# Optimization experiments

Hardware: AMD Instinct MI355X
Metric: run time of the kernel (lower is better)

## Reference

```python
import jax, jax.numpy as jnp
import numpy as np

B, S, D_IN, D_OUT, H = 4, 2048, 1024, 1024, 16
HD = D_OUT // H


def setup_inputs() -> dict:
    key = jax.random.key(0)
    ks = jax.random.split(key, 6)
    sc_in = 1.0 / np.sqrt(D_IN)
    sc_out = 1.0 / np.sqrt(D_OUT)
    return {
        "x": jax.random.normal(ks[0], (B, S, D_IN), dtype=jnp.float32),
        "Wq": jax.random.normal(ks[1], (D_IN, D_OUT), dtype=jnp.float32) * sc_in,
        "Wk": jax.random.normal(ks[2], (D_IN, D_OUT), dtype=jnp.float32) * sc_in,
        "Wv": jax.random.normal(ks[3], (D_IN, D_OUT), dtype=jnp.float32) * sc_in,
        "Wo": jax.random.normal(ks[4], (D_OUT, D_OUT), dtype=jnp.float32) * sc_out,
        "bo": jax.random.normal(ks[5], (D_OUT,), dtype=jnp.float32) * 0.01,
    }


def reference(x, Wq, Wk, Wv, Wo, bo):
    b, s, _ = x.shape
    # projections -> [b, h, s, hd]
    def split_heads(t):
        return t.reshape(b, s, H, HD).transpose(0, 2, 1, 3)
    q = split_heads(x @ Wq)
    k = split_heads(x @ Wk)
    v = split_heads(x @ Wv)
    # full score matrix [b, h, s, s], causal mask, scaled softmax
    scores = jnp.einsum("bhqd,bhkd->bhqk", q, k)
    causal = jnp.tril(jnp.ones((s, s), dtype=bool))
    scores = jnp.where(causal, scores, -jnp.inf)
    attn = jax.nn.softmax(scores / np.sqrt(HD), axis=-1)
    # dropout p=0.0 -> identity
    ctx = jnp.einsum("bhqk,bhkd->bhqd", attn, v)
    ctx = ctx.transpose(0, 2, 1, 3).reshape(b, s, D_OUT)
    return ctx @ Wo + bo
```

## Files before the change

kernel.cpp:

```cpp
#include <hip/hip_runtime.h>


typedef float  f32x4  __attribute__((ext_vector_type(4)));
typedef __bf16 bf16x8 __attribute__((ext_vector_type(8)));
typedef __bf16 bf16x4 __attribute__((ext_vector_type(4)));

#define AS(n) __attribute__((address_space(n)))

__device__ __forceinline__ void gload16(const void* g, void* l) {
    __builtin_amdgcn_global_load_lds((const AS(1) void*)g, (AS(3) void*)l, 16, 0, 0);
}

__device__ __forceinline__ f32x4 mfma16(bf16x8 a, bf16x8 b, f32x4 c) {
    return __builtin_amdgcn_mfma_f32_16x16x32_bf16(a, b, c, 0, 0, 0);
}

__global__ void prep_kernel(const float4* __restrict__ x, __bf16* __restrict__ xb,
                            const float* __restrict__ Wq, const float* __restrict__ Wk,
                            const float* __restrict__ Wv, const float* __restrict__ Wo,
                            __bf16* __restrict__ wqkvt, __bf16* __restrict__ wot) {
    __shared__ float tile[32][33];
    int bid = blockIdx.x, tid = threadIdx.x;
    if (bid < 8192) {
        int t = bid * 256 + tid;
        float4 v = x[t];
        bf16x4 o = { (__bf16)v.x, (__bf16)v.y, (__bf16)v.z, (__bf16)v.w };
        ((bf16x4*)xb)[t] = o;
        return;
    }
    int idx = bid - 8192;
    int z = idx >> 10, rest = idx & 1023;
    int by = rest >> 5, bx = rest & 31;
    const float* src; __bf16* dst;
    if (z == 0)      { src = Wq; dst = wqkvt; }
    else if (z == 1) { src = Wk; dst = wqkvt + 1048576; }
    else if (z == 2) { src = Wv; dst = wqkvt + 2097152; }
    else             { src = Wo; dst = wot; }
    int tx = tid & 31, ty = tid >> 5;
    int xcol = bx * 32 + tx;
    int y0 = by * 32;
#pragma unroll
    for (int i = ty; i < 32; i += 8) tile[i][tx] = src[(size_t)(y0 + i) * 1024 + xcol];
    __syncthreads();
    int xo = by * 32 + tx;
    int yo0 = bx * 32;
#pragma unroll
    for (int i = ty; i < 32; i += 8) dst[(size_t)(yo0 + i) * 1024 + xo] = (__bf16)tile[tx][i];
}

__global__ __launch_bounds__(256, 2) void gemm_qkv_kernel(
        const __bf16* __restrict__ A, const __bf16* __restrict__ Bt,
        __bf16* __restrict__ Qp, __bf16* __restrict__ Kp, __bf16* __restrict__ Vt) {
    __shared__ __bf16 lA[128 * 32];
    __shared__ __bf16 lB[128 * 32];
    __shared__ __bf16 lT[128 * 136];
    int tid = threadIdx.x;
    int m0 = blockIdx.x * 128, n0 = blockIdx.y * 128;
    int w = tid >> 6, lane = tid & 63, quad = lane >> 4, l15 = lane & 15;
    int wm = (w & 1) * 64, wn = (w >> 1) * 64;
    f32x4 acc[4][4] = {};
    int rowS = tid >> 2, kc = tid & 3;
    const __bf16* Abase = A + (size_t)m0 * 1024;
    const __bf16* Bbase = Bt + (size_t)n0 * 1024;
    for (int kt = 0; kt < 32; kt++) {
        int k0 = kt * 32;
        gload16(Abase + (size_t)rowS * 1024 + k0 + kc * 8,        &lA[tid * 8]);
        gload16(Abase + (size_t)(rowS + 64) * 1024 + k0 + kc * 8, &lA[(tid + 256) * 8]);
        gload16(Bbase + (size_t)rowS * 1024 + k0 + kc * 8,        &lB[tid * 8]);
        gload16(Bbase + (size_t)(rowS + 64) * 1024 + k0 + kc * 8, &lB[(tid + 256) * 8]);
        __syncthreads();
        bf16x8 a[4], b[4];
#pragma unroll
        for (int i = 0; i < 4; i++) a[i] = *(const bf16x8*)&lA[(wm + i * 16 + l15) * 32 + quad * 8];
#pragma unroll
        for (int j = 0; j < 4; j++) b[j] = *(const bf16x8*)&lB[(wn + j * 16 + l15) * 32 + quad * 8];
#pragma unroll
        for (int i = 0; i < 4; i++)
#pragma unroll
            for (int j = 0; j < 4; j++)
                acc[i][j] = mfma16(a[i], b[j], acc[i][j]);
        __syncthreads();
    }
    int mat = n0 >> 10;
    int ncol0 = n0 & 1023;
    if (mat < 2) {
        __bf16* dst = (mat == 0) ? Qp : Kp;
        float sc = (mat == 0) ? 0.1803368801111204f : 1.0f;
#pragma unroll
        for (int i = 0; i < 4; i++) {
#pragma unroll
            for (int j = 0; j < 4; j++) {
                int n = ncol0 + wn + j * 16 + l15;
                int h = n >> 6, d = n & 63;
#pragma unroll
                for (int r = 0; r < 4; r++) {
                    int m = m0 + wm + i * 16 + quad * 4 + r;
                    int bb = m >> 11, s = m & 2047;
                    dst[((((size_t)bb * 16 + h) * 2048 + s) << 6) + d] = (__bf16)(acc[i][j][r] * sc);
                }
            }
        }
    } else {
#pragma unroll
        for (int i = 0; i < 4; i++)
#pragma unroll
            for (int j = 0; j < 4; j++)
#pragma unroll
                for (int r = 0; r < 4; r++)
                    lT[(wn + j * 16 + l15) * 136 + wm + i * 16 + quad * 4 + r] = (__bf16)acc[i][j][r];
        __syncthreads();
        int row = tid >> 1, c0 = (tid & 1) * 64;
        int n = ncol0 + row;
        int hh = n >> 6, d = n & 63;
        int bb = m0 >> 11, s0 = (m0 & 2047) + c0;
        __bf16* dst = Vt + (((size_t)(bb * 16 + hh)) * 64 + d) * 2048 + s0;
#pragma unroll
        for (int e = 0; e < 8; e++)
            *(bf16x8*)(dst + e * 8) = *(const bf16x8*)&lT[row * 136 + c0 + e * 8];
    }
}

__global__ __launch_bounds__(256, 3) void attn_kernel(
        const __bf16* __restrict__ Q, const __bf16* __restrict__ K,
        const __bf16* __restrict__ Vt, __bf16* __restrict__ ctx) {
    int bid = blockIdx.x;
    int qx = bid >> 6;
    int bh = bid & 63;
    int qt = 15 - qx;
    int b = bh >> 4, h = bh & 15;
    const __bf16* Qb = Q  + (size_t)bh * (2048 * 64);
    const __bf16* Kb = K  + (size_t)bh * (2048 * 64);
    const __bf16* Vb = Vt + (size_t)bh * (64 * 2048);
    __shared__ __bf16 sK[2][64 * 72];
    __shared__ __bf16 sV[2][64 * 72];
    __shared__ __bf16 sP[64 * 72];
    int tid = threadIdx.x, w = tid >> 6, lane = tid & 63, quad = lane >> 4, l15 = lane & 15;
    int srow = tid >> 2, scol = tid & 3;
    int vd = tid >> 2, vc = tid & 3;
    const bf16x8 vone = { (__bf16)1.0f, (__bf16)1.0f, (__bf16)1.0f, (__bf16)1.0f,
                          (__bf16)1.0f, (__bf16)1.0f, (__bf16)1.0f, (__bf16)1.0f };

    int q0 = qt * 128;
    int nkt = 2 * qt + 2;
    bf16x8 aQ[2][2];
#pragma unroll
    for (int h2 = 0; h2 < 2; h2++)
#pragma unroll
        for (int c = 0; c < 2; c++)
            aQ[h2][c] = *(const bf16x8*)(Qb + (size_t)(q0 + w * 32 + h2 * 16 + l15) * 64 + c * 32 + quad * 8);
    f32x4 o[2][4] = {};
    f32x4 lac[2] = {};
    {
        const __bf16* kp = Kb + srow * 64 + scol * 16;
        const __bf16* vp = Vb + (size_t)vd * 2048 + vc * 16;
        bf16x8 kA = *(const bf16x8*)kp;
        bf16x8 kB = *(const bf16x8*)(kp + 8);
        bf16x8 vA = *(const bf16x8*)vp;
        bf16x8 vB = *(const bf16x8*)(vp + 8);
        *(bf16x8*)&sK[0][srow * 72 + scol * 16]     = kA;
        *(bf16x8*)&sK[0][srow * 72 + scol * 16 + 8] = kB;
        *(bf16x8*)&sV[0][vd * 72 + vc * 16]         = vA;
        *(bf16x8*)&sV[0][vd * 72 + vc * 16 + 8]     = vB;
    }
    for (int kt = 0; kt < nkt; kt++) {
        int cur = kt & 1;
        __syncthreads();
        bf16x8 kA, kB, vA, vB;
        if (kt + 1 < nkt) {
            const __bf16* kp = Kb + ((kt + 1) * 64 + srow) * 64 + scol * 16;
            const __bf16* vp = Vb + (size_t)vd * 2048 + (kt + 1) * 64 + vc * 16;
            kA = *(const bf16x8*)kp;  kB = *(const bf16x8*)(kp + 8);
            vA = *(const bf16x8*)vp;  vB = *(const bf16x8*)(vp + 8);
        }
        int mb = kt * 64 - q0;
        bool diag = (kt >= 2 * qt);
        if (!(diag && (mb - w * 32 >= 32))) {
            f32x4 s[2][4] = {};
            __builtin_amdgcn_s_setprio(1);
#pragma unroll
            for (int c = 0; c < 2; c++)
#pragma unroll
                for (int j = 0; j < 4; j++) {
                    bf16x8 kf = *(const bf16x8*)&sK[cur][(j * 16 + l15) * 72 + c * 32 + quad * 8];
                    s[0][j] = mfma16(aQ[0][c], kf, s[0][j]);
                    s[1][j] = mfma16(aQ[1][c], kf, s[1][j]);
                }
            __builtin_amdgcn_s_setprio(0);
            if (diag && (mb + 63 > w * 32)) {
#pragma unroll
                for (int h2 = 0; h2 < 2; h2++)
#pragma unroll
                    for (int j = 0; j < 4; j++) {
                        int key = j * 16 + l15 + mb;
#pragma unroll
                        for (int r = 0; r < 4; r++)
                            if (key > w * 32 + h2 * 16 + quad * 4 + r) s[h2][j][r] = -1e30f;
                    }
            }
#pragma unroll
            for (int h2 = 0; h2 < 2; h2++)
#pragma unroll
                for (int j = 0; j < 4; j++)
#pragma unroll
                    for (int r = 0; r < 4; r++)
                        s[h2][j][r] = exp2f(s[h2][j][r]);
            bf16x8 vv0[4], vv1[4];
#pragma unroll
            for (int dj = 0; dj < 4; dj++) {
                int vrow = (dj * 16 + l15) * 72;
                vv0[dj] = *(const bf16x8*)&sV[cur][vrow + quad * 8];
                vv1[dj] = *(const bf16x8*)&sV[cur][vrow + quad * 8 + 32];
            }
            int pswz = (l15 >> 2) << 4;
#pragma unroll
            for (int h2 = 0; h2 < 2; h2++) {
#pragma unroll
                for (int j = 0; j < 4; j++) {
                    int kg = ((j ^ quad) << 4) + l15;
#pragma unroll
                    for (int r = 0; r < 4; r++)
                        sP[(w * 16 + quad * 4 + r) * 72 + kg] = (__bf16)s[h2][j][r];
                }
                int prow = (w * 16 + l15) * 72;
                bf16x8 p0 = *(const bf16x8*)&sP[prow + ((quad * 8) ^ pswz)];
                bf16x8 p1 = *(const bf16x8*)&sP[prow + ((quad * 8 + 32) ^ pswz)];
                __builtin_amdgcn_s_setprio(1);
                lac[h2] = mfma16(p0, vone, lac[h2]);
                lac[h2] = mfma16(p1, vone, lac[h2]);
#pragma unroll
                for (int dj = 0; dj < 4; dj++) {
                    f32x4 tt = mfma16(p0, vv0[dj], o[h2][dj]);
                    o[h2][dj] = mfma16(p1, vv1[dj], tt);
                }
                __builtin_amdgcn_s_setprio(0);
            }
        }
        if (kt + 1 < nkt) {
            *(bf16x8*)&sK[1 - cur][srow * 72 + scol * 16]     = kA;
            *(bf16x8*)&sK[1 - cur][srow * 72 + scol * 16 + 8] = kB;
            *(bf16x8*)&sV[1 - cur][vd * 72 + vc * 16]         = vA;
            *(bf16x8*)&sV[1 - cur][vd * 72 + vc * 16 + 8]     = vB;
        }
    }
#pragma unroll
    for (int h2 = 0; h2 < 2; h2++)
#pragma unroll
        for (int r = 0; r < 4; r++) {
            float inv = 1.0f / lac[h2][r];
            int q = q0 + w * 32 + h2 * 16 + quad * 4 + r;
            size_t base = (((size_t)b * 2048 + q) << 10) + h * 64;
#pragma unroll
            for (int dj = 0; dj < 4; dj++)
                ctx[base + dj * 16 + l15] = (__bf16)(o[h2][dj][r] * inv);
        }
}

__global__ __launch_bounds__(256, 2) void gemm_out_kernel(
        const __bf16* __restrict__ A, const __bf16* __restrict__ Bt,
        const float* __restrict__ bo, float* __restrict__ out) {
    __shared__ __bf16 lA[128 * 32];
    __shared__ __bf16 lB[128 * 32];
    int tid = threadIdx.x;
    int m0 = blockIdx.x * 128, n0 = blockIdx.y * 128;
    int w = tid >> 6, lane = tid & 63, quad = lane >> 4, l15 = lane & 15;
    int wm = (w & 1) * 64, wn = (w >> 1) * 64;
    f32x4 acc[4][4] = {};
    int rowS = tid >> 2, kc = tid & 3;
    const __bf16* Abase = A + (size_t)m0 * 1024;
    const __bf16* Bbase = Bt + (size_t)n0 * 1024;
    for (int kt = 0; kt < 32; kt++) {
        int k0 = kt * 32;
        gload16(Abase + (size_t)rowS * 1024 + k0 + kc * 8,        &lA[tid * 8]);
        gload16(Abase + (size_t)(rowS + 64) * 1024 + k0 + kc * 8, &lA[(tid + 256) * 8]);
        gload16(Bbase + (size_t)rowS * 1024 + k0 + kc * 8,        &lB[tid * 8]);
        gload16(Bbase + (size_t)(rowS + 64) * 1024 + k0 + kc * 8, &lB[(tid + 256) * 8]);
        __syncthreads();
        bf16x8 a[4], b[4];
#pragma unroll
        for (int i = 0; i < 4; i++) a[i] = *(const bf16x8*)&lA[(wm + i * 16 + l15) * 32 + quad * 8];
#pragma unroll
        for (int j = 0; j < 4; j++) b[j] = *(const bf16x8*)&lB[(wn + j * 16 + l15) * 32 + quad * 8];
#pragma unroll
        for (int i = 0; i < 4; i++)
#pragma unroll
            for (int j = 0; j < 4; j++)
                acc[i][j] = mfma16(a[i], b[j], acc[i][j]);
        __syncthreads();
    }
#pragma unroll
    for (int j = 0; j < 4; j++) {
        int n = n0 + wn + j * 16 + l15;
        float bias = bo[n];
#pragma unroll
        for (int i = 0; i < 4; i++)
#pragma unroll
            for (int r = 0; r < 4; r++) {
                int m = m0 + wm + i * 16 + quad * 4 + r;
                out[(size_t)m * 1024 + n] = acc[i][j][r] + bias;
            }
    }
}

extern "C" void kernel_launch(void* const* d_in, const int* in_sizes, int n_in,
                              void* d_out, int out_size, void* d_ws, size_t ws_size,
                              hipStream_t stream) {
    const float* x  = (const float*)d_in[0];
    const float* Wq = (const float*)d_in[1];
    const float* Wk = (const float*)d_in[2];
    const float* Wv = (const float*)d_in[3];
    const float* Wo = (const float*)d_in[4];
    const float* bo = (const float*)d_in[5];
    float* out = (float*)d_out;

    __bf16* ws    = (__bf16*)d_ws;
    __bf16* xb    = ws;
    __bf16* wqkvt = xb + 8388608;
    __bf16* wot   = wqkvt + 3145728;
    __bf16* Qp    = wot + 1048576;
    __bf16* Kp    = Qp + 8388608;
    __bf16* Vt    = Kp + 8388608;
    __bf16* ctx   = Vt + 8388608;

    prep_kernel<<<12288, 256, 0, stream>>>((const float4*)x, xb, Wq, Wk, Wv, Wo, wqkvt, wot);
    gemm_qkv_kernel<<<dim3(64, 24), 256, 0, stream>>>(xb, wqkvt, Qp, Kp, Vt);
    attn_kernel<<<1024, 256, 0, stream>>>(Qp, Kp, Vt, ctx);
    gemm_out_kernel<<<dim3(64, 8), 256, 0, stream>>>(ctx, wot, bo, out);
}
```

Baseline: 250.0 us.

## Compute transposed scores to feed P directly from registers, drop sP LDS round-trip

```diff
diff --git a/kernel.cpp b/kernel.cpp
--- a/kernel.cpp
+++ b/kernel.cpp
@@ -120,7 +120,7 @@
     }
 }
 
-__global__ __launch_bounds__(256, 3) void attn_kernel(
+__global__ __launch_bounds__(256, 4) void attn_kernel(
         const __bf16* __restrict__ Q, const __bf16* __restrict__ K,
         const __bf16* __restrict__ Vt, __bf16* __restrict__ ctx) {
     int bid = blockIdx.x;
@@ -133,10 +133,10 @@
     const __bf16* Vb = Vt + (size_t)bh * (64 * 2048);
     __shared__ __bf16 sK[2][64 * 72];
     __shared__ __bf16 sV[2][64 * 72];
-    __shared__ __bf16 sP[64 * 72];
     int tid = threadIdx.x, w = tid >> 6, lane = tid & 63, quad = lane >> 4, l15 = lane & 15;
     int srow = tid >> 2, scol = tid & 3;
     int vd = tid >> 2, vc = tid & 3;
+    int vbase = vd * 72 + (vc >> 1) * 32 + (vc & 1) * 4;
     const bf16x8 vone = { (__bf16)1.0f, (__bf16)1.0f, (__bf16)1.0f, (__bf16)1.0f,
                           (__bf16)1.0f, (__bf16)1.0f, (__bf16)1.0f, (__bf16)1.0f };
 
@@ -159,8 +159,10 @@
         bf16x8 vB = *(const bf16x8*)(vp + 8);
         *(bf16x8*)&sK[0][srow * 72 + scol * 16]     = kA;
         *(bf16x8*)&sK[0][srow * 72 + scol * 16 + 8] = kB;
-        *(bf16x8*)&sV[0][vd * 72 + vc * 16]         = vA;
-        *(bf16x8*)&sV[0][vd * 72 + vc * 16 + 8]     = vB;
+        *(bf16x4*)&sV[0][vbase]      = __builtin_shufflevector(vA, vA, 0, 1, 2, 3);
+        *(bf16x4*)&sV[0][vbase + 8]  = __builtin_shufflevector(vA, vA, 4, 5, 6, 7);
+        *(bf16x4*)&sV[0][vbase + 16] = __builtin_shufflevector(vB, vB, 0, 1, 2, 3);
+        *(bf16x4*)&sV[0][vbase + 24] = __builtin_shufflevector(vB, vB, 4, 5, 6, 7);
     }
     for (int kt = 0; kt < nkt; kt++) {
         int cur = kt & 1;
@@ -175,27 +177,28 @@
         int mb = kt * 64 - q0;
         bool diag = (kt >= 2 * qt);
         if (!(diag && (mb - w * 32 >= 32))) {
-            f32x4 s[2][4] = {};
+            f32x4 sT[2][4] = {};
             __builtin_amdgcn_s_setprio(1);
 #pragma unroll
             for (int c = 0; c < 2; c++)
 #pragma unroll
                 for (int j = 0; j < 4; j++) {
                     bf16x8 kf = *(const bf16x8*)&sK[cur][(j * 16 + l15) * 72 + c * 32 + quad * 8];
-                    s[0][j] = mfma16(aQ[0][c], kf, s[0][j]);
-                    s[1][j] = mfma16(aQ[1][c], kf, s[1][j]);
+                    sT[0][j] = mfma16(kf, aQ[0][c], sT[0][j]);
+                    sT[1][j] = mfma16(kf, aQ[1][c], sT[1][j]);
                 }
             __builtin_amdgcn_s_setprio(0);
             if (diag && (mb + 63 > w * 32)) {
 #pragma unroll
-                for (int h2 = 0; h2 < 2; h2++)
+                for (int h2 = 0; h2 < 2; h2++) {
+                    int qrow = w * 32 + h2 * 16 + l15;
 #pragma unroll
                     for (int j = 0; j < 4; j++) {
-                        int key = j * 16 + l15 + mb;
 #pragma unroll
                         for (int r = 0; r < 4; r++)
-                            if (key > w * 32 + h2 * 16 + quad * 4 + r) s[h2][j][r] = -1e30f;
+                            if (j * 16 + quad * 4 + r + mb > qrow) sT[h2][j][r] = -1e30f;
                     }
+                }
             }
 #pragma unroll
             for (int h2 = 0; h2 < 2; h2++)
@@ -203,7 +206,7 @@
                 for (int j = 0; j < 4; j++)
 #pragma unroll
                     for (int r = 0; r < 4; r++)
-                        s[h2][j][r] = exp2f(s[h2][j][r]);
+                        sT[h2][j][r] = exp2f(sT[h2][j][r]);
             bf16x8 vv0[4], vv1[4];
 #pragma unroll
             for (int dj = 0; dj < 4; dj++) {
@@ -211,26 +214,23 @@
                 vv0[dj] = *(const bf16x8*)&sV[cur][vrow + quad * 8];
                 vv1[dj] = *(const bf16x8*)&sV[cur][vrow + quad * 8 + 32];
             }
-            int pswz = (l15 >> 2) << 4;
 #pragma unroll
             for (int h2 = 0; h2 < 2; h2++) {
-#pragma unroll
-                for (int j = 0; j < 4; j++) {
-                    int kg = ((j ^ quad) << 4) + l15;
-#pragma unroll
-                    for (int r = 0; r < 4; r++)
-                        sP[(w * 16 + quad * 4 + r) * 72 + kg] = (__bf16)s[h2][j][r];
-                }
-                int prow = (w * 16 + l15) * 72;
-                bf16x8 p0 = *(const bf16x8*)&sP[prow + ((quad * 8) ^ pswz)];
-                bf16x8 p1 = *(const bf16x8*)&sP[prow + ((quad * 8 + 32) ^ pswz)];
+                bf16x8 pA0, pA1;
+#pragma unroll
+                for (int e = 0; e < 4; e++) {
+                    pA0[e]     = (__bf16)sT[h2][0][e];
+                    pA0[e + 4] = (__bf16)sT[h2][1][e];
+                    pA1[e]     = (__bf16)sT[h2][2][e];
+                    pA1[e + 4] = (__bf16)sT[h2][3][e];
+                }
                 __builtin_amdgcn_s_setprio(1);
-                lac[h2] = mfma16(p0, vone, lac[h2]);
-                lac[h2] = mfma16(p1, vone, lac[h2]);
+                lac[h2] = mfma16(pA0, vone, lac[h2]);
+                lac[h2] = mfma16(pA1, vone, lac[h2]);
 #pragma unroll
                 for (int dj = 0; dj < 4; dj++) {
-                    f32x4 tt = mfma16(p0, vv0[dj], o[h2][dj]);
-                    o[h2][dj] = mfma16(p1, vv1[dj], tt);
+                    f32x4 tt = mfma16(pA0, vv0[dj], o[h2][dj]);
+                    o[h2][dj] = mfma16(pA1, vv1[dj], tt);
                 }
                 __builtin_amdgcn_s_setprio(0);
             }
@@ -238,8 +238,10 @@
         if (kt + 1 < nkt) {
             *(bf16x8*)&sK[1 - cur][srow * 72 + scol * 16]     = kA;
             *(bf16x8*)&sK[1 - cur][srow * 72 + scol * 16 + 8] = kB;
-            *(bf16x8*)&sV[1 - cur][vd * 72 + vc * 16]         = vA;
-            *(bf16x8*)&sV[1 - cur][vd * 72 + vc * 16 + 8]     = vB;
+            *(bf16x4*)&sV[1 - cur][vbase]      = __builtin_shufflevector(vA, vA, 0, 1, 2, 3);
+            *(bf16x4*)&sV[1 - cur][vbase + 8]  = __builtin_shufflevector(vA, vA, 4, 5, 6, 7);
+            *(bf16x4*)&sV[1 - cur][vbase + 16] = __builtin_shufflevector(vB, vB, 0, 1, 2, 3);
+            *(bf16x4*)&sV[1 - cur][vbase + 24] = __builtin_shufflevector(vB, vB, 4, 5, 6, 7);
         }
     }
 #pragma unroll
```

Result: slower. 314.1 us (+25.6%).
